# Performance work log

Hardware: AMD Instinct MI355X
Metric: run time of the kernel (lower is better)

## Reference

```python
import jax, jax.numpy as jnp
import numpy as np

SORB = 64      # spin orbitals (sequence length)
NELE = 32      # electrons
H = 512        # num_hiddens
B = 4096       # batch
ALPHA = NELE // 2                      # = beta = 16 (spin-up / spin-down electrons)
MIN_I = min(SORB - 2 * ALPHA, 2 * ALPHA)  # = 32; symmetry mask active for i >= MIN_I
EPS = 1e-12


def setup_inputs() -> dict:
    key = jax.random.key(0)
    ks = jax.random.split(key, 10)
    s_in = 1.0 / np.sqrt(2.0)
    s_h = 1.0 / np.sqrt(H)
    return {
        "x": jax.random.randint(ks[0], (B, SORB), 0, 2, dtype=jnp.int32),  # occupancies {0,1}
        "W_ih0": jax.random.normal(ks[1], (3 * H, 2), jnp.float32) * s_in,   # GRU layer0 input weights (r,z,n)
        "W_hh0": jax.random.normal(ks[2], (3 * H, H), jnp.float32) * s_h,
        "W_ih1": jax.random.normal(ks[3], (3 * H, H), jnp.float32) * s_h,    # GRU layer1
        "W_hh1": jax.random.normal(ks[4], (3 * H, H), jnp.float32) * s_h,
        "W_amp": jax.random.normal(ks[5], (2, H), jnp.float32) * s_h,
        "b_amp": jax.random.normal(ks[6], (2,), jnp.float32) * 0.01,
        "W_phase": jax.random.normal(ks[7], (2, H), jnp.float32) * s_h,
        "b_phase": jax.random.normal(ks[8], (2,), jnp.float32) * 0.01,
    }


def _gru_cell(x_in, h, Wih, Whh):
    # PyTorch GRU (bias=False), gate order r, z, n
    gi = x_in @ Wih.T          # (B, 3H)
    gh = h @ Whh.T             # (B, 3H)
    r = jax.nn.sigmoid(gi[:, :H] + gh[:, :H])
    z = jax.nn.sigmoid(gi[:, H:2 * H] + gh[:, H:2 * H])
    n = jnp.tanh(gi[:, 2 * H:] + r * gh[:, 2 * H:])
    return (1.0 - z) * n + z * h


def reference(x, W_ih0, W_hh0, W_ih1, W_hh1, W_amp, b_amp, W_phase, b_phase):
    dt = W_ih0.dtype
    bits = x.astype(jnp.int32)           # (B, SORB) occupancies
    nb = bits.shape[0]

    def step(carry, inp):
        h0, h1, x0, amp, phase, nup, ndn = carry
        i, b_i = inp                      # site index, occupancy bits (B,)
        h0n = _gru_cell(x0, h0, W_ih0, W_hh0)
        h1n = _gru_cell(h0n, h1, W_ih1, W_hh1)
        y = h1n                           # (B, H)
        # amplitude: sqrt(softmax(linear))
        y_amp = jnp.sqrt(jax.nn.softmax(y @ W_amp.T + b_amp, axis=1))   # (B, 2)
        # phase: pi * softsign(linear)
        ph = y @ W_phase.T + b_phase
        y_ph = jnp.pi * ph / (1.0 + jnp.abs(ph))
        # particle-number symmetry mask (alpha == beta spin sectors)
        is_even = (i % 2) == 0            # even sites: spin-up, odd: spin-down
        cnt = jnp.where(is_even, nup, ndn)
        lower = (ALPHA - SORB // 2 + i // 2).astype(dt)
        occ_ok = (cnt < ALPHA).astype(dt)
        unocc_ok = (cnt > lower).astype(dt)
        mask = jnp.stack([unocc_ok, occ_ok], axis=1)
        masked = y_amp * mask
        masked = masked / jnp.sqrt(jnp.sum(masked * masked, axis=1, keepdims=True) + EPS)
        y_amp = jnp.where(i >= MIN_I, masked, y_amp)
        # accumulate conditional amplitude / phase at the sampled occupancy
        sel_a = jnp.take_along_axis(y_amp, b_i[:, None], axis=1)[:, 0]
        sel_p = jnp.take_along_axis(y_ph, b_i[:, None], axis=1)[:, 0]
        amp = amp * sel_a
        phase = phase + sel_p
        bf = b_i.astype(dt)
        nup = nup + jnp.where(is_even, bf, 0.0)
        ndn = ndn + jnp.where(is_even, 0.0, bf)
        x0n = jax.nn.one_hot(b_i, 2, dtype=dt)  # next-step GRU input
        return (h0n, h1n, x0n, amp, phase, nup, ndn), None

    init = (
        jnp.zeros((nb, H), dt), jnp.zeros((nb, H), dt), jnp.zeros((nb, 2), dt),
        jnp.ones((nb,), dt), jnp.zeros((nb,), dt), jnp.zeros((nb,), dt), jnp.zeros((nb,), dt),
    )
    xs = (jnp.arange(SORB), bits.T)       # scan over sites
    (_, _, _, amp, phase, _, _), _ = jax.lax.scan(step, init, xs)
    # complex wavefunction psi = amp * exp(1j*phase); returned as real pair (amp, phase)
    return jnp.stack([amp, phase], axis=-1)
```

## Files before the change

### kernel.cpp

```cpp
#include <hip/hip_runtime.h>
#include <hip/hip_bf16.h>

#define SORB  64
#define HID   512
#define BATCH 4096
#define N3H   1536
#define KD    512
#define BK    64
#define PI_F  3.14159265358979f

typedef _Float16 half8 __attribute__((ext_vector_type(8)));
typedef float    floatx4 __attribute__((ext_vector_type(4)));

__device__ __forceinline__ void gload16(const void* g, void* l) {
    __builtin_amdgcn_global_load_lds(
        (const __attribute__((address_space(1))) void*)g,
        (__attribute__((address_space(3))) void*)l, 16, 0, 0);
}

__device__ __forceinline__ float sigmoidf_(float x) { return 1.f / (1.f + __expf(-x)); }
__device__ __forceinline__ float tanhf_(float x) {
    x = fminf(fmaxf(x, -15.f), 15.f);
    const float e2 = __expf(2.f * x);
    return (e2 - 1.f) / (e2 + 1.f);
}

__global__ __launch_bounds__(256) void convw_kernel(
    const float* __restrict__ w0, const float* __restrict__ w1, const float* __restrict__ w2,
    _Float16* __restrict__ o0, _Float16* __restrict__ o1, _Float16* __restrict__ o2)
{
    const int i = blockIdx.x * 256 + threadIdx.x;
    if (i < N3H * KD) {
        o0[i] = (_Float16)w0[i];
        o1[i] = (_Float16)w1[i];
        o2[i] = (_Float16)w2[i];
    }
}

__global__ __launch_bounds__(256) void init_kernel(
    float* __restrict__ amp, float* __restrict__ phase,
    int* __restrict__ nup, int* __restrict__ ndn)
{
    const int i = blockIdx.x * 256 + threadIdx.x;
    if (i < BATCH) { amp[i] = 1.f; phase[i] = 0.f; nup[i] = 0; ndn[i] = 0; }
}


__global__ __launch_bounds__(256) void step1_kernel(
    const _Float16* __restrict__ h0h_c, const _Float16* __restrict__ h1h_c,
    const _Float16* __restrict__ wh0,   const _Float16* __restrict__ wh1,
    const float* __restrict__ Wih0, const int* __restrict__ bits,
    float* __restrict__ h0f, _Float16* __restrict__ h0h_n,
    _Float16* __restrict__ gB, int step)
{
    const int z = blockIdx.z;
    const _Float16* A = z ? h1h_c : h0h_c;
    const _Float16* W = z ? wh1 : wh0;
    const int j0 = blockIdx.x * 64;
    const int m0 = blockIdx.y * 64;

    __shared__ __align__(16) _Float16 As[64 * BK];
    __shared__ __align__(16) _Float16 Bs[192 * BK];

    const int tid  = threadIdx.x;
    const int lane = tid & 63;
    const int wid  = tid >> 6;
    const int wm   = wid >> 1, wj = wid & 1;

    floatx4 acc[2][2][3];
    const floatx4 z4 = {0.f, 0.f, 0.f, 0.f};
#pragma unroll
    for (int a = 0; a < 2; ++a)
#pragma unroll
        for (int b = 0; b < 2; ++b)
#pragma unroll
            for (int g = 0; g < 3; ++g) acc[a][b][g] = z4;

    const _Float16* a_srcp[2];
#pragma unroll
    for (int k2 = 0; k2 < 2; ++k2) {
        const int p = tid + k2 * 256, row = p >> 3, c = (p & 7) ^ (row & 7);
        a_srcp[k2] = A + (size_t)(m0 + row) * KD + c * 8;
    }
    const _Float16* b_srcp[6];
#pragma unroll
    for (int k2 = 0; k2 < 6; ++k2) {
        const int p = tid + k2 * 256, row = p >> 3, c = (p & 7) ^ (row & 7);
        const int grow = (row >> 6) * HID + j0 + (row & 63);
        b_srcp[k2] = W + (size_t)grow * KD + c * 8;
    }
    _Float16* a_dst[2];
#pragma unroll
    for (int k2 = 0; k2 < 2; ++k2) a_dst[k2] = As + (size_t)(k2 * 256 + wid * 64) * 8;
    _Float16* b_dst[6];
#pragma unroll
    for (int k2 = 0; k2 < 6; ++k2) b_dst[k2] = Bs + (size_t)(k2 * 256 + wid * 64) * 8;

    const int ku = lane >> 4;
    int aoff[2][2], boff[2][3][2];
#pragma unroll
    for (int mf = 0; mf < 2; ++mf) {
        const int r = wm * 32 + mf * 16 + (lane & 15);
#pragma unroll
        for (int kk = 0; kk < 2; ++kk)
            aoff[mf][kk] = r * BK + (((kk * 4 + ku) ^ (r & 7)) * 8);
    }
#pragma unroll
    for (int jf = 0; jf < 2; ++jf)
#pragma unroll
        for (int g = 0; g < 3; ++g) {
            const int r = g * 64 + wj * 32 + jf * 16 + (lane & 15);
#pragma unroll
            for (int kk = 0; kk < 2; ++kk)
                boff[jf][g][kk] = r * BK + (((kk * 4 + ku) ^ (r & 7)) * 8);
        }

    for (int kt = 0; kt < 8; ++kt) {
        const int k0 = kt * BK;
#pragma unroll
        for (int k2 = 0; k2 < 2; ++k2) gload16(a_srcp[k2] + k0, a_dst[k2]);
#pragma unroll
        for (int k2 = 0; k2 < 6; ++k2) gload16(b_srcp[k2] + k0, b_dst[k2]);
        __syncthreads();
#pragma unroll
        for (int kk = 0; kk < 2; ++kk) {
            half8 af[2], bf[2][3];
#pragma unroll
            for (int mf = 0; mf < 2; ++mf) af[mf] = *(const half8*)(As + aoff[mf][kk]);
#pragma unroll
            for (int jf = 0; jf < 2; ++jf)
#pragma unroll
                for (int g = 0; g < 3; ++g) bf[jf][g] = *(const half8*)(Bs + boff[jf][g][kk]);
#pragma unroll
            for (int mf = 0; mf < 2; ++mf)
#pragma unroll
                for (int jf = 0; jf < 2; ++jf)
#pragma unroll
                    for (int g = 0; g < 3; ++g)
                        acc[mf][jf][g] = __builtin_amdgcn_mfma_f32_16x16x32_f16(af[mf], bf[jf][g], acc[mf][jf][g], 0, 0, 0);
        }
        __syncthreads();
    }

    if (z == 0) {
#pragma unroll
        for (int mf = 0; mf < 2; ++mf)
#pragma unroll
            for (int jf = 0; jf < 2; ++jf) {
                const floatx4 gr = acc[mf][jf][0];
                const floatx4 gz = acc[mf][jf][1];
                const floatx4 gn = acc[mf][jf][2];
#pragma unroll
                for (int reg = 0; reg < 4; ++reg) {
                    const int m = m0 + wm * 32 + mf * 16 + (lane >> 4) * 4 + reg;
                    const int j = j0 + wj * 32 + jf * 16 + (lane & 15);
                    float gir = 0.f, giz = 0.f, gin = 0.f;
                    if (step > 0) {
                        const int t = bits[m * SORB + step - 1];
                        gir = Wih0[j * 2 + t];
                        giz = Wih0[(HID + j) * 2 + t];
                        gin = Wih0[(2 * HID + j) * 2 + t];
                    }
                    const float r  = sigmoidf_(gir + gr[reg]);
                    const float zz = sigmoidf_(giz + gz[reg]);
                    const float n  = tanhf_(gin + r * gn[reg]);
                    const size_t idx = (size_t)m * HID + j;
                    const float h  = h0f[idx];
                    const float hn = (1.f - zz) * n + zz * h;
                    h0f[idx]   = hn;
                    h0h_n[idx] = (_Float16)hn;
                }
            }
    } else {
#pragma unroll
        for (int mf = 0; mf < 2; ++mf)
#pragma unroll
            for (int jf = 0; jf < 2; ++jf)
#pragma unroll
                for (int g = 0; g < 3; ++g)
#pragma unroll
                    for (int reg = 0; reg < 4; ++reg) {
                        const int m = m0 + wm * 32 + mf * 16 + (lane >> 4) * 4 + reg;
                        const int j = j0 + wj * 32 + jf * 16 + (lane & 15);
                        gB[(size_t)m * N3H + g * HID + j] = (_Float16)acc[mf][jf][g][reg];
                    }
    }
}

__global__ __launch_bounds__(256) void step2_kernel(
    const _Float16* __restrict__ h0h_n, const _Float16* __restrict__ wi1,
    const _Float16* __restrict__ gB,
    float* __restrict__ h1f, _Float16* __restrict__ h1h_n)
{
    const int j0 = blockIdx.x * 64;
    const int m0 = blockIdx.y * 64;

    __shared__ __align__(16) _Float16 As[64 * BK];
    __shared__ __align__(16) _Float16 Bs[192 * BK];

    const int tid  = threadIdx.x;
    const int lane = tid & 63;
    const int wid  = tid >> 6;
    const int wm   = wid >> 1, wj = wid & 1;

    floatx4 acc[2][2][3];
    const floatx4 z4 = {0.f, 0.f, 0.f, 0.f};
#pragma unroll
    for (int a = 0; a < 2; ++a)
#pragma unroll
        for (int b = 0; b < 2; ++b)
#pragma unroll
            for (int g = 0; g < 3; ++g) acc[a][b][g] = z4;

    const _Float16* a_srcp[2];
#pragma unroll
    for (int k2 = 0; k2 < 2; ++k2) {
        const int p = tid + k2 * 256, row = p >> 3, c = (p & 7) ^ (row & 7);
        a_srcp[k2] = h0h_n + (size_t)(m0 + row) * KD + c * 8;
    }
    const _Float16* b_srcp[6];
#pragma unroll
    for (int k2 = 0; k2 < 6; ++k2) {
        const int p = tid + k2 * 256, row = p >> 3, c = (p & 7) ^ (row & 7);
        const int grow = (row >> 6) * HID + j0 + (row & 63);
        b_srcp[k2] = wi1 + (size_t)grow * KD + c * 8;
    }
    _Float16* a_dst[2];
#pragma unroll
    for (int k2 = 0; k2 < 2; ++k2) a_dst[k2] = As + (size_t)(k2 * 256 + wid * 64) * 8;
    _Float16* b_dst[6];
#pragma unroll
    for (int k2 = 0; k2 < 6; ++k2) b_dst[k2] = Bs + (size_t)(k2 * 256 + wid * 64) * 8;

    const int ku = lane >> 4;
    int aoff[2][2], boff[2][3][2];
#pragma unroll
    for (int mf = 0; mf < 2; ++mf) {
        const int r = wm * 32 + mf * 16 + (lane & 15);
#pragma unroll
        for (int kk = 0; kk < 2; ++kk)
            aoff[mf][kk] = r * BK + (((kk * 4 + ku) ^ (r & 7)) * 8);
    }
#pragma unroll
    for (int jf = 0; jf < 2; ++jf)
#pragma unroll
        for (int g = 0; g < 3; ++g) {
            const int r = g * 64 + wj * 32 + jf * 16 + (lane & 15);
#pragma unroll
            for (int kk = 0; kk < 2; ++kk)
                boff[jf][g][kk] = r * BK + (((kk * 4 + ku) ^ (r & 7)) * 8);
        }

    for (int kt = 0; kt < 8; ++kt) {
        const int k0 = kt * BK;
#pragma unroll
        for (int k2 = 0; k2 < 2; ++k2) gload16(a_srcp[k2] + k0, a_dst[k2]);
#pragma unroll
        for (int k2 = 0; k2 < 6; ++k2) gload16(b_srcp[k2] + k0, b_dst[k2]);
        __syncthreads();
#pragma unroll
        for (int kk = 0; kk < 2; ++kk) {
            half8 af[2], bf[2][3];
#pragma unroll
            for (int mf = 0; mf < 2; ++mf) af[mf] = *(const half8*)(As + aoff[mf][kk]);
#pragma unroll
            for (int jf = 0; jf < 2; ++jf)
#pragma unroll
                for (int g = 0; g < 3; ++g) bf[jf][g] = *(const half8*)(Bs + boff[jf][g][kk]);
#pragma unroll
            for (int mf = 0; mf < 2; ++mf)
#pragma unroll
                for (int jf = 0; jf < 2; ++jf)
#pragma unroll
                    for (int g = 0; g < 3; ++g)
                        acc[mf][jf][g] = __builtin_amdgcn_mfma_f32_16x16x32_f16(af[mf], bf[jf][g], acc[mf][jf][g], 0, 0, 0);
        }
        __syncthreads();
    }

#pragma unroll
    for (int mf = 0; mf < 2; ++mf)
#pragma unroll
        for (int jf = 0; jf < 2; ++jf) {
            const floatx4 gr = acc[mf][jf][0];
            const floatx4 gz = acc[mf][jf][1];
            const floatx4 gn = acc[mf][jf][2];
#pragma unroll
            for (int reg = 0; reg < 4; ++reg) {
                const int m = m0 + wm * 32 + mf * 16 + (lane >> 4) * 4 + reg;
                const int j = j0 + wj * 32 + jf * 16 + (lane & 15);
                const size_t gbase = (size_t)m * N3H;
                const float ghr = (float)gB[gbase + j];
                const float ghz = (float)gB[gbase + HID + j];
                const float ghn = (float)gB[gbase + 2 * HID + j];
                const float r  = sigmoidf_(gr[reg] + ghr);
                const float zz = sigmoidf_(gz[reg] + ghz);
                const float n  = tanhf_(gn[reg] + r * ghn);
                const size_t idx = (size_t)m * HID + j;
                const float h  = h1f[idx];
                const float hn = (1.f - zz) * n + zz * h;
                h1f[idx]   = hn;
                h1h_n[idx] = (_Float16)hn;
            }
        }
}

__global__ __launch_bounds__(256) void head_kernel(
    const _Float16* __restrict__ h1h_n,
    const float* __restrict__ Wamp, const float* __restrict__ bamp,
    const float* __restrict__ Wph,  const float* __restrict__ bph,
    const int* __restrict__ bits,
    float* __restrict__ amp, float* __restrict__ phase,
    int* __restrict__ nup, int* __restrict__ ndn,
    float* __restrict__ out, int step)
{
    const int lane = threadIdx.x & 63;
    const int m    = blockIdx.x * 4 + (threadIdx.x >> 6);
    const half8 hv = *(const half8*)(h1h_n + (size_t)m * HID + lane * 8);
    float d0 = 0.f, d1 = 0.f, d2 = 0.f, d3 = 0.f;
#pragma unroll
    for (int e = 0; e < 8; ++e) {
        const int j = lane * 8 + e;
        const float hn = (float)hv[e];
        d0 += hn * Wamp[j];       d1 += hn * Wamp[HID + j];
        d2 += hn * Wph[j];        d3 += hn * Wph[HID + j];
    }
#pragma unroll
    for (int off = 1; off < 64; off <<= 1) {
        d0 += __shfl_xor(d0, off); d1 += __shfl_xor(d1, off);
        d2 += __shfl_xor(d2, off); d3 += __shfl_xor(d3, off);
    }
    if (lane == 0) {
        const float a0 = d0 + bamp[0];
        const float a1 = d1 + bamp[1];
        const float mx = fmaxf(a0, a1);
        const float e0 = __expf(a0 - mx), e1 = __expf(a1 - mx);
        const float inv = 1.f / (e0 + e1);
        float ya0 = sqrtf(e0 * inv), ya1 = sqrtf(e1 * inv);
        const float p0 = d2 + bph[0];
        const float p1 = d3 + bph[1];
        const float yp0 = PI_F * p0 / (1.f + fabsf(p0));
        const float yp1 = PI_F * p1 / (1.f + fabsf(p1));
        const int even = ((step & 1) == 0);
        const int cnt = even ? nup[m] : ndn[m];
        if (step >= 32) {
            const int lower = (step >> 1) - 16;
            const float m0v = (cnt > lower) ? ya0 : 0.f;
            const float m1v = (cnt < 16) ? ya1 : 0.f;
            const float nrm = sqrtf(m0v * m0v + m1v * m1v + 1e-12f);
            ya0 = m0v / nrm; ya1 = m1v / nrm;
        }
        const int bi = bits[m * SORB + step];
        const float na = amp[m] * (bi ? ya1 : ya0);
        const float np = phase[m] + (bi ? yp1 : yp0);
        amp[m] = na; phase[m] = np;
        if (bi) { if (even) nup[m] = cnt + 1; else ndn[m] = cnt + 1; }
        if (step == SORB - 1) {
            out[m * 2 + 0] = na;
            out[m * 2 + 1] = np;
        }
    }
}

extern "C" void kernel_launch(void* const* d_in, const int* in_sizes, int n_in,
                              void* d_out, int out_size, void* d_ws, size_t ws_size,
                              hipStream_t stream) {
    const int*   bits = (const int*)d_in[0];
    const float* Wih0 = (const float*)d_in[1];
    const float* Whh0 = (const float*)d_in[2];
    const float* Wih1 = (const float*)d_in[3];
    const float* Whh1 = (const float*)d_in[4];
    const float* Wamp = (const float*)d_in[5];
    const float* bamp = (const float*)d_in[6];
    const float* Wph  = (const float*)d_in[7];
    const float* bph  = (const float*)d_in[8];
    float* out = (float*)d_out;

    char* ws = (char*)d_ws;
    size_t off = 0;
    auto alloc = [&](size_t bytes) {
        void* p = ws + off;
        off = (off + bytes + 255) & ~(size_t)255;
        return p;
    };
    _Float16* wh0 = (_Float16*)alloc((size_t)N3H * KD * 2);
    _Float16* wi1 = (_Float16*)alloc((size_t)N3H * KD * 2);
    _Float16* wh1 = (_Float16*)alloc((size_t)N3H * KD * 2);
    float*    h0f = (float*)alloc((size_t)BATCH * HID * 4);
    float*    h1f = (float*)alloc((size_t)BATCH * HID * 4);
    _Float16* h0hA = (_Float16*)alloc((size_t)BATCH * HID * 2);
    _Float16* h0hB = (_Float16*)alloc((size_t)BATCH * HID * 2);
    _Float16* h1hA = (_Float16*)alloc((size_t)BATCH * HID * 2);
    _Float16* h1hB = (_Float16*)alloc((size_t)BATCH * HID * 2);
    _Float16* gB  = (_Float16*)alloc((size_t)BATCH * N3H * 2);
    float*    amp   = (float*)alloc((size_t)BATCH * 4);
    float*    phase = (float*)alloc((size_t)BATCH * 4);
    int*      nup   = (int*)alloc((size_t)BATCH * 4);
    int*      ndn   = (int*)alloc((size_t)BATCH * 4);

    _Float16* h0h[2] = {h0hA, h0hB};
    _Float16* h1h[2] = {h1hA, h1hB};

    hipMemsetAsync(h0f, 0, (size_t)BATCH * HID * 4, stream);
    hipMemsetAsync(h1f, 0, (size_t)BATCH * HID * 4, stream);
    hipMemsetAsync(h0hA, 0, (size_t)BATCH * HID * 2, stream);
    hipMemsetAsync(h1hA, 0, (size_t)BATCH * HID * 2, stream);
    convw_kernel<<<(N3H * KD + 255) / 256, 256, 0, stream>>>(Whh0, Wih1, Whh1, wh0, wi1, wh1);
    init_kernel<<<BATCH / 256, 256, 0, stream>>>(amp, phase, nup, ndn);

    for (int s = 0; s < SORB; ++s) {
        const int cur = s & 1, nxt = cur ^ 1;
        step1_kernel<<<dim3(8, 64, 2), 256, 0, stream>>>(
            h0h[cur], h1h[cur], wh0, wh1, Wih0, bits, h0f, h0h[nxt], gB, s);
        step2_kernel<<<dim3(8, 64, 1), 256, 0, stream>>>(
            h0h[nxt], wi1, gB, h1f, h1h[nxt]);
        head_kernel<<<BATCH / 4, 256, 0, stream>>>(
            h1h[nxt], Wamp, bamp, Wph, bph, bits, amp, phase, nup, ndn, out, s);
    }
}
```

Before: 3.307 ms.

## Fuse head into next step's GEMM, double-buffer weights, load A directly to registers

The per-step head kernel is folded into the z=1 blocks of the next step1 launch, which process the previous step's h1 rows. A single head launch remains at the end for the last step, which removes one launch per step. The GEMM kernels now double-buffer the weight tile in LDS so the next tile's load overlaps the current MFMAs, and they read the activation operand straight from global memory into registers instead of staging it in LDS. The costs are larger LDS use (two 24KB buffers), which may lower occupancy, and extra epilogue work in the z=1 blocks.

```diff
diff --git a/kernel.cpp b/kernel.cpp
--- a/kernel.cpp
+++ b/kernel.cpp
@@ -45,278 +45,16 @@
     if (i < BATCH) { amp[i] = 1.f; phase[i] = 0.f; nup[i] = 0; ndn[i] = 0; }
 }
 
-
-__global__ __launch_bounds__(256) void step1_kernel(
-    const _Float16* __restrict__ h0h_c, const _Float16* __restrict__ h1h_c,
-    const _Float16* __restrict__ wh0,   const _Float16* __restrict__ wh1,
-    const float* __restrict__ Wih0, const int* __restrict__ bits,
-    float* __restrict__ h0f, _Float16* __restrict__ h0h_n,
-    _Float16* __restrict__ gB, int step)
-{
-    const int z = blockIdx.z;
-    const _Float16* A = z ? h1h_c : h0h_c;
-    const _Float16* W = z ? wh1 : wh0;
-    const int j0 = blockIdx.x * 64;
-    const int m0 = blockIdx.y * 64;
-
-    __shared__ __align__(16) _Float16 As[64 * BK];
-    __shared__ __align__(16) _Float16 Bs[192 * BK];
-
-    const int tid  = threadIdx.x;
-    const int lane = tid & 63;
-    const int wid  = tid >> 6;
-    const int wm   = wid >> 1, wj = wid & 1;
-
-    floatx4 acc[2][2][3];
-    const floatx4 z4 = {0.f, 0.f, 0.f, 0.f};
-#pragma unroll
-    for (int a = 0; a < 2; ++a)
-#pragma unroll
-        for (int b = 0; b < 2; ++b)
-#pragma unroll
-            for (int g = 0; g < 3; ++g) acc[a][b][g] = z4;
-
-    const _Float16* a_srcp[2];
-#pragma unroll
-    for (int k2 = 0; k2 < 2; ++k2) {
-        const int p = tid + k2 * 256, row = p >> 3, c = (p & 7) ^ (row & 7);
-        a_srcp[k2] = A + (size_t)(m0 + row) * KD + c * 8;
-    }
-    const _Float16* b_srcp[6];
-#pragma unroll
-    for (int k2 = 0; k2 < 6; ++k2) {
-        const int p = tid + k2 * 256, row = p >> 3, c = (p & 7) ^ (row & 7);
-        const int grow = (row >> 6) * HID + j0 + (row & 63);
-        b_srcp[k2] = W + (size_t)grow * KD + c * 8;
-    }
-    _Float16* a_dst[2];
-#pragma unroll
-    for (int k2 = 0; k2 < 2; ++k2) a_dst[k2] = As + (size_t)(k2 * 256 + wid * 64) * 8;
-    _Float16* b_dst[6];
-#pragma unroll
-    for (int k2 = 0; k2 < 6; ++k2) b_dst[k2] = Bs + (size_t)(k2 * 256 + wid * 64) * 8;
-
-    const int ku = lane >> 4;
-    int aoff[2][2], boff[2][3][2];
-#pragma unroll
-    for (int mf = 0; mf < 2; ++mf) {
-        const int r = wm * 32 + mf * 16 + (lane & 15);
-#pragma unroll
-        for (int kk = 0; kk < 2; ++kk)
-            aoff[mf][kk] = r * BK + (((kk * 4 + ku) ^ (r & 7)) * 8);
-    }
-#pragma unroll
-    for (int jf = 0; jf < 2; ++jf)
-#pragma unroll
-        for (int g = 0; g < 3; ++g) {
-            const int r = g * 64 + wj * 32 + jf * 16 + (lane & 15);
-#pragma unroll
-            for (int kk = 0; kk < 2; ++kk)
-                boff[jf][g][kk] = r * BK + (((kk * 4 + ku) ^ (r & 7)) * 8);
-        }
-
-    for (int kt = 0; kt < 8; ++kt) {
-        const int k0 = kt * BK;
-#pragma unroll
-        for (int k2 = 0; k2 < 2; ++k2) gload16(a_srcp[k2] + k0, a_dst[k2]);
-#pragma unroll
-        for (int k2 = 0; k2 < 6; ++k2) gload16(b_srcp[k2] + k0, b_dst[k2]);
-        __syncthreads();
-#pragma unroll
-        for (int kk = 0; kk < 2; ++kk) {
-            half8 af[2], bf[2][3];
-#pragma unroll
-            for (int mf = 0; mf < 2; ++mf) af[mf] = *(const half8*)(As + aoff[mf][kk]);
-#pragma unroll
-            for (int jf = 0; jf < 2; ++jf)
-#pragma unroll
-                for (int g = 0; g < 3; ++g) bf[jf][g] = *(const half8*)(Bs + boff[jf][g][kk]);
-#pragma unroll
-            for (int mf = 0; mf < 2; ++mf)
-#pragma unroll
-                for (int jf = 0; jf < 2; ++jf)
-#pragma unroll
-                    for (int g = 0; g < 3; ++g)
-                        acc[mf][jf][g] = __builtin_amdgcn_mfma_f32_16x16x32_f16(af[mf], bf[jf][g], acc[mf][jf][g], 0, 0, 0);
-        }
-        __syncthreads();
-    }
-
-    if (z == 0) {
-#pragma unroll
-        for (int mf = 0; mf < 2; ++mf)
-#pragma unroll
-            for (int jf = 0; jf < 2; ++jf) {
-                const floatx4 gr = acc[mf][jf][0];
-                const floatx4 gz = acc[mf][jf][1];
-                const floatx4 gn = acc[mf][jf][2];
-#pragma unroll
-                for (int reg = 0; reg < 4; ++reg) {
-                    const int m = m0 + wm * 32 + mf * 16 + (lane >> 4) * 4 + reg;
-                    const int j = j0 + wj * 32 + jf * 16 + (lane & 15);
-                    float gir = 0.f, giz = 0.f, gin = 0.f;
-                    if (step > 0) {
-                        const int t = bits[m * SORB + step - 1];
-                        gir = Wih0[j * 2 + t];
-                        giz = Wih0[(HID + j) * 2 + t];
-                        gin = Wih0[(2 * HID + j) * 2 + t];
-                    }
-                    const float r  = sigmoidf_(gir + gr[reg]);
-                    const float zz = sigmoidf_(giz + gz[reg]);
-                    const float n  = tanhf_(gin + r * gn[reg]);
-                    const size_t idx = (size_t)m * HID + j;
-                    const float h  = h0f[idx];
-                    const float hn = (1.f - zz) * n + zz * h;
-                    h0f[idx]   = hn;
-                    h0h_n[idx] = (_Float16)hn;
-                }
-            }
-    } else {
-#pragma unroll
-        for (int mf = 0; mf < 2; ++mf)
-#pragma unroll
-            for (int jf = 0; jf < 2; ++jf)
-#pragma unroll
-                for (int g = 0; g < 3; ++g)
-#pragma unroll
-                    for (int reg = 0; reg < 4; ++reg) {
-                        const int m = m0 + wm * 32 + mf * 16 + (lane >> 4) * 4 + reg;
-                        const int j = j0 + wj * 32 + jf * 16 + (lane & 15);
-                        gB[(size_t)m * N3H + g * HID + j] = (_Float16)acc[mf][jf][g][reg];
-                    }
-    }
-}
-
-__global__ __launch_bounds__(256) void step2_kernel(
-    const _Float16* __restrict__ h0h_n, const _Float16* __restrict__ wi1,
-    const _Float16* __restrict__ gB,
-    float* __restrict__ h1f, _Float16* __restrict__ h1h_n)
-{
-    const int j0 = blockIdx.x * 64;
-    const int m0 = blockIdx.y * 64;
-
-    __shared__ __align__(16) _Float16 As[64 * BK];
-    __shared__ __align__(16) _Float16 Bs[192 * BK];
-
-    const int tid  = threadIdx.x;
-    const int lane = tid & 63;
-    const int wid  = tid >> 6;
-    const int wm   = wid >> 1, wj = wid & 1;
-
-    floatx4 acc[2][2][3];
-    const floatx4 z4 = {0.f, 0.f, 0.f, 0.f};
-#pragma unroll
-    for (int a = 0; a < 2; ++a)
-#pragma unroll
-        for (int b = 0; b < 2; ++b)
-#pragma unroll
-            for (int g = 0; g < 3; ++g) acc[a][b][g] = z4;
-
-    const _Float16* a_srcp[2];
-#pragma unroll
-    for (int k2 = 0; k2 < 2; ++k2) {
-        const int p = tid + k2 * 256, row = p >> 3, c = (p & 7) ^ (row & 7);
-        a_srcp[k2] = h0h_n + (size_t)(m0 + row) * KD + c * 8;
-    }
-    const _Float16* b_srcp[6];
-#pragma unroll
-    for (int k2 = 0; k2 < 6; ++k2) {
-        const int p = tid + k2 * 256, row = p >> 3, c = (p & 7) ^ (row & 7);
-        const int grow = (row >> 6) * HID + j0 + (row & 63);
-        b_srcp[k2] = wi1 + (size_t)grow * KD + c * 8;
-    }
-    _Float16* a_dst[2];
-#pragma unroll
-    for (int k2 = 0; k2 < 2; ++k2) a_dst[k2] = As + (size_t)(k2 * 256 + wid * 64) * 8;
-    _Float16* b_dst[6];
-#pragma unroll
-    for (int k2 = 0; k2 < 6; ++k2) b_dst[k2] = Bs + (size_t)(k2 * 256 + wid * 64) * 8;
-
-    const int ku = lane >> 4;
-    int aoff[2][2], boff[2][3][2];
-#pragma unroll
-    for (int mf = 0; mf < 2; ++mf) {
-        const int r = wm * 32 + mf * 16 + (lane & 15);
-#pragma unroll
-        for (int kk = 0; kk < 2; ++kk)
-            aoff[mf][kk] = r * BK + (((kk * 4 + ku) ^ (r & 7)) * 8);
-    }
-#pragma unroll
-    for (int jf = 0; jf < 2; ++jf)
-#pragma unroll
-        for (int g = 0; g < 3; ++g) {
-            const int r = g * 64 + wj * 32 + jf * 16 + (lane & 15);
-#pragma unroll
-            for (int kk = 0; kk < 2; ++kk)
-                boff[jf][g][kk] = r * BK + (((kk * 4 + ku) ^ (r & 7)) * 8);
-        }
-
-    for (int kt = 0; kt < 8; ++kt) {
-        const int k0 = kt * BK;
-#pragma unroll
-        for (int k2 = 0; k2 < 2; ++k2) gload16(a_srcp[k2] + k0, a_dst[k2]);
-#pragma unroll
-        for (int k2 = 0; k2 < 6; ++k2) gload16(b_srcp[k2] + k0, b_dst[k2]);
-        __syncthreads();
-#pragma unroll
-        for (int kk = 0; kk < 2; ++kk) {
-            half8 af[2], bf[2][3];
-#pragma unroll
-            for (int mf = 0; mf < 2; ++mf) af[mf] = *(const half8*)(As + aoff[mf][kk]);
-#pragma unroll
-            for (int jf = 0; jf < 2; ++jf)
-#pragma unroll
-                for (int g = 0; g < 3; ++g) bf[jf][g] = *(const half8*)(Bs + boff[jf][g][kk]);
-#pragma unroll
-            for (int mf = 0; mf < 2; ++mf)
-#pragma unroll
-                for (int jf = 0; jf < 2; ++jf)
-#pragma unroll
-                    for (int g = 0; g < 3; ++g)
-                        acc[mf][jf][g] = __builtin_amdgcn_mfma_f32_16x16x32_f16(af[mf], bf[jf][g], acc[mf][jf][g], 0, 0, 0);
-        }
-        __syncthreads();
-    }
-
-#pragma unroll
-    for (int mf = 0; mf < 2; ++mf)
-#pragma unroll
-        for (int jf = 0; jf < 2; ++jf) {
-            const floatx4 gr = acc[mf][jf][0];
-            const floatx4 gz = acc[mf][jf][1];
-            const floatx4 gn = acc[mf][jf][2];
-#pragma unroll
-            for (int reg = 0; reg < 4; ++reg) {
-                const int m = m0 + wm * 32 + mf * 16 + (lane >> 4) * 4 + reg;
-                const int j = j0 + wj * 32 + jf * 16 + (lane & 15);
-                const size_t gbase = (size_t)m * N3H;
-                const float ghr = (float)gB[gbase + j];
-                const float ghz = (float)gB[gbase + HID + j];
-                const float ghn = (float)gB[gbase + 2 * HID + j];
-                const float r  = sigmoidf_(gr[reg] + ghr);
-                const float zz = sigmoidf_(gz[reg] + ghz);
-                const float n  = tanhf_(gn[reg] + r * ghn);
-                const size_t idx = (size_t)m * HID + j;
-                const float h  = h1f[idx];
-                const float hn = (1.f - zz) * n + zz * h;
-                h1f[idx]   = hn;
-                h1h_n[idx] = (_Float16)hn;
-            }
-        }
-}
-
-__global__ __launch_bounds__(256) void head_kernel(
-    const _Float16* __restrict__ h1h_n,
+__device__ __forceinline__ void head_row(
+    const _Float16* __restrict__ h1, int m,
     const float* __restrict__ Wamp, const float* __restrict__ bamp,
     const float* __restrict__ Wph,  const float* __restrict__ bph,
     const int* __restrict__ bits,
     float* __restrict__ amp, float* __restrict__ phase,
     int* __restrict__ nup, int* __restrict__ ndn,
-    float* __restrict__ out, int step)
-{
-    const int lane = threadIdx.x & 63;
-    const int m    = blockIdx.x * 4 + (threadIdx.x >> 6);
-    const half8 hv = *(const half8*)(h1h_n + (size_t)m * HID + lane * 8);
+    float* __restrict__ out, int step, int lane)
+{
+    const half8 hv = *(const half8*)(h1 + (size_t)m * HID + lane * 8);
     float d0 = 0.f, d1 = 0.f, d2 = 0.f, d3 = 0.f;
 #pragma unroll
     for (int e = 0; e < 8; ++e) {
@@ -360,6 +98,296 @@
             out[m * 2 + 1] = np;
         }
     }
+}
+
+__global__ __launch_bounds__(256) void step1_kernel(
+    const _Float16* __restrict__ h0h_c, const _Float16* __restrict__ h1h_c,
+    const _Float16* __restrict__ wh0,   const _Float16* __restrict__ wh1,
+    const float* __restrict__ Wih0, const int* __restrict__ bits,
+    float* __restrict__ h0f, _Float16* __restrict__ h0h_n,
+    _Float16* __restrict__ gB, int step,
+    const float* __restrict__ Wamp, const float* __restrict__ bamp,
+    const float* __restrict__ Wph,  const float* __restrict__ bph,
+    float* __restrict__ amp, float* __restrict__ phase,
+    int* __restrict__ nup, int* __restrict__ ndn, float* __restrict__ out)
+{
+    const int z = blockIdx.z;
+    const _Float16* Aop = z ? h1h_c : h0h_c;
+    const _Float16* Wop = z ? wh1 : wh0;
+    const int j0 = blockIdx.x * 64;
+    const int m0 = blockIdx.y * 64;
+
+    __shared__ __align__(16) _Float16 Bs[2][192 * BK];
+
+    const int tid  = threadIdx.x;
+    const int lane = tid & 63;
+    const int wid  = tid >> 6;
+    const int wm   = wid >> 1, wj = wid & 1;
+    const int ku   = lane >> 4;
+
+    floatx4 acc[2][2][3];
+    const floatx4 z4 = {0.f, 0.f, 0.f, 0.f};
+#pragma unroll
+    for (int a = 0; a < 2; ++a)
+#pragma unroll
+        for (int b = 0; b < 2; ++b)
+#pragma unroll
+            for (int g = 0; g < 3; ++g) acc[a][b][g] = z4;
+
+    const _Float16* b_srcp[6];
+#pragma unroll
+    for (int k2 = 0; k2 < 6; ++k2) {
+        const int p = tid + k2 * 256, row = p >> 3, c = (p & 7) ^ (row & 7);
+        const int grow = (row >> 6) * HID + j0 + (row & 63);
+        b_srcp[k2] = Wop + (size_t)grow * KD + c * 8;
+    }
+    _Float16* b_dst0[6];
+    _Float16* b_dst1[6];
+#pragma unroll
+    for (int k2 = 0; k2 < 6; ++k2) {
+        b_dst0[k2] = Bs[0] + (size_t)(k2 * 256 + wid * 64) * 8;
+        b_dst1[k2] = Bs[1] + (size_t)(k2 * 256 + wid * 64) * 8;
+    }
+
+    const _Float16* a_row[2];
+#pragma unroll
+    for (int mf = 0; mf < 2; ++mf)
+        a_row[mf] = Aop + (size_t)(m0 + wm * 32 + mf * 16 + (lane & 15)) * KD + ku * 8;
+
+    int boff[2][3][2];
+#pragma unroll
+    for (int jf = 0; jf < 2; ++jf)
+#pragma unroll
+        for (int g = 0; g < 3; ++g) {
+            const int r = g * 64 + wj * 32 + jf * 16 + (lane & 15);
+#pragma unroll
+            for (int kk = 0; kk < 2; ++kk)
+                boff[jf][g][kk] = r * BK + (((kk * 4 + ku) ^ (r & 7)) * 8);
+        }
+
+#pragma unroll
+    for (int k2 = 0; k2 < 6; ++k2) gload16(b_srcp[k2], b_dst0[k2]);
+    __syncthreads();
+
+#pragma unroll
+    for (int kt = 0; kt < 8; ++kt) {
+        half8 af[2][2];
+#pragma unroll
+        for (int mf = 0; mf < 2; ++mf)
+#pragma unroll
+            for (int kk = 0; kk < 2; ++kk)
+                af[mf][kk] = *(const half8*)(a_row[mf] + kt * BK + kk * 32);
+        if (kt < 7) {
+#pragma unroll
+            for (int k2 = 0; k2 < 6; ++k2)
+                gload16(b_srcp[k2] + (kt + 1) * BK, ((kt & 1) ? b_dst0 : b_dst1)[k2]);
+        }
+        const _Float16* Bcur = Bs[kt & 1];
+#pragma unroll
+        for (int kk = 0; kk < 2; ++kk) {
+            half8 bf[2][3];
+#pragma unroll
+            for (int jf = 0; jf < 2; ++jf)
+#pragma unroll
+                for (int g = 0; g < 3; ++g) bf[jf][g] = *(const half8*)(Bcur + boff[jf][g][kk]);
+#pragma unroll
+            for (int mf = 0; mf < 2; ++mf)
+#pragma unroll
+                for (int jf = 0; jf < 2; ++jf)
+#pragma unroll
+                    for (int g = 0; g < 3; ++g)
+                        acc[mf][jf][g] = __builtin_amdgcn_mfma_f32_16x16x32_f16(
+                            af[mf][kk], bf[jf][g], acc[mf][jf][g], 0, 0, 0);
+        }
+        __syncthreads();
+    }
+
+    if (z == 0) {
+#pragma unroll
+        for (int mf = 0; mf < 2; ++mf)
+#pragma unroll
+            for (int jf = 0; jf < 2; ++jf) {
+                const floatx4 gr = acc[mf][jf][0];
+                const floatx4 gz = acc[mf][jf][1];
+                const floatx4 gn = acc[mf][jf][2];
+#pragma unroll
+                for (int reg = 0; reg < 4; ++reg) {
+                    const int m = m0 + wm * 32 + mf * 16 + (lane >> 4) * 4 + reg;
+                    const int j = j0 + wj * 32 + jf * 16 + (lane & 15);
+                    float gir = 0.f, giz = 0.f, gin = 0.f;
+                    if (step > 0) {
+                        const int tb = bits[m * SORB + step - 1];
+                        gir = Wih0[j * 2 + tb];
+                        giz = Wih0[(HID + j) * 2 + tb];
+                        gin = Wih0[(2 * HID + j) * 2 + tb];
+                    }
+                    const float r  = sigmoidf_(gir + gr[reg]);
+                    const float zz = sigmoidf_(giz + gz[reg]);
+                    const float n  = tanhf_(gin + r * gn[reg]);
+                    const size_t idx = (size_t)m * HID + j;
+                    const float h  = h0f[idx];
+                    const float hn = (1.f - zz) * n + zz * h;
+                    h0f[idx]   = hn;
+                    h0h_n[idx] = (_Float16)hn;
+                }
+            }
+    } else {
+#pragma unroll
+        for (int mf = 0; mf < 2; ++mf)
+#pragma unroll
+            for (int jf = 0; jf < 2; ++jf)
+#pragma unroll
+                for (int g = 0; g < 3; ++g)
+#pragma unroll
+                    for (int reg = 0; reg < 4; ++reg) {
+                        const int m = m0 + wm * 32 + mf * 16 + (lane >> 4) * 4 + reg;
+                        const int j = j0 + wj * 32 + jf * 16 + (lane & 15);
+                        gB[(size_t)m * N3H + g * HID + j] = (_Float16)acc[mf][jf][g][reg];
+                    }
+        if (step > 0) {
+            const int bid = blockIdx.y * 8 + blockIdx.x;
+#pragma unroll
+            for (int rr = 0; rr < 2; ++rr) {
+                const int m = bid * 8 + wid * 2 + rr;
+                head_row(h1h_c, m, Wamp, bamp, Wph, bph, bits,
+                         amp, phase, nup, ndn, out, step - 1, lane);
+            }
+        }
+    }
+}
+
+__global__ __launch_bounds__(256) void step2_kernel(
+    const _Float16* __restrict__ h0h_n, const _Float16* __restrict__ wi1,
+    const _Float16* __restrict__ gB,
+    float* __restrict__ h1f, _Float16* __restrict__ h1h_n)
+{
+    const int j0 = blockIdx.x * 64;
+    const int m0 = blockIdx.y * 64;
+
+    __shared__ __align__(16) _Float16 Bs[2][192 * BK];
+
+    const int tid  = threadIdx.x;
+    const int lane = tid & 63;
+    const int wid  = tid >> 6;
+    const int wm   = wid >> 1, wj = wid & 1;
+    const int ku   = lane >> 4;
+
+    floatx4 acc[2][2][3];
+    const floatx4 z4 = {0.f, 0.f, 0.f, 0.f};
+#pragma unroll
+    for (int a = 0; a < 2; ++a)
+#pragma unroll
+        for (int b = 0; b < 2; ++b)
+#pragma unroll
+            for (int g = 0; g < 3; ++g) acc[a][b][g] = z4;
+
+    const _Float16* b_srcp[6];
+#pragma unroll
+    for (int k2 = 0; k2 < 6; ++k2) {
+        const int p = tid + k2 * 256, row = p >> 3, c = (p & 7) ^ (row & 7);
+        const int grow = (row >> 6) * HID + j0 + (row & 63);
+        b_srcp[k2] = wi1 + (size_t)grow * KD + c * 8;
+    }
+    _Float16* b_dst0[6];
+    _Float16* b_dst1[6];
+#pragma unroll
+    for (int k2 = 0; k2 < 6; ++k2) {
+        b_dst0[k2] = Bs[0] + (size_t)(k2 * 256 + wid * 64) * 8;
+        b_dst1[k2] = Bs[1] + (size_t)(k2 * 256 + wid * 64) * 8;
+    }
+
+    const _Float16* a_row[2];
+#pragma unroll
+    for (int mf = 0; mf < 2; ++mf)
+        a_row[mf] = h0h_n + (size_t)(m0 + wm * 32 + mf * 16 + (lane & 15)) * KD + ku * 8;
+
+    int boff[2][3][2];
+#pragma unroll
+    for (int jf = 0; jf < 2; ++jf)
+#pragma unroll
+        for (int g = 0; g < 3; ++g) {
+            const int r = g * 64 + wj * 32 + jf * 16 + (lane & 15);
+#pragma unroll
+            for (int kk = 0; kk < 2; ++kk)
+                boff[jf][g][kk] = r * BK + (((kk * 4 + ku) ^ (r & 7)) * 8);
+        }
+
+#pragma unroll
+    for (int k2 = 0; k2 < 6; ++k2) gload16(b_srcp[k2], b_dst0[k2]);
+    __syncthreads();
+
+#pragma unroll
+    for (int kt = 0; kt < 8; ++kt) {
+        half8 af[2][2];
+#pragma unroll
+        for (int mf = 0; mf < 2; ++mf)
+#pragma unroll
+            for (int kk = 0; kk < 2; ++kk)
+                af[mf][kk] = *(const half8*)(a_row[mf] + kt * BK + kk * 32);
+        if (kt < 7) {
+#pragma unroll
+            for (int k2 = 0; k2 < 6; ++k2)
+                gload16(b_srcp[k2] + (kt + 1) * BK, ((kt & 1) ? b_dst0 : b_dst1)[k2]);
+        }
+        const _Float16* Bcur = Bs[kt & 1];
+#pragma unroll
+        for (int kk = 0; kk < 2; ++kk) {
+            half8 bf[2][3];
+#pragma unroll
+            for (int jf = 0; jf < 2; ++jf)
+#pragma unroll
+                for (int g = 0; g < 3; ++g) bf[jf][g] = *(const half8*)(Bcur + boff[jf][g][kk]);
+#pragma unroll
+            for (int mf = 0; mf < 2; ++mf)
+#pragma unroll
+                for (int jf = 0; jf < 2; ++jf)
+#pragma unroll
+                    for (int g = 0; g < 3; ++g)
+                        acc[mf][jf][g] = __builtin_amdgcn_mfma_f32_16x16x32_f16(
+                            af[mf][kk], bf[jf][g], acc[mf][jf][g], 0, 0, 0);
+        }
+        __syncthreads();
+    }
+
+#pragma unroll
+    for (int mf = 0; mf < 2; ++mf)
+#pragma unroll
+        for (int jf = 0; jf < 2; ++jf) {
+            const floatx4 gr = acc[mf][jf][0];
+            const floatx4 gz = acc[mf][jf][1];
+            const floatx4 gn = acc[mf][jf][2];
+#pragma unroll
+            for (int reg = 0; reg < 4; ++reg) {
+                const int m = m0 + wm * 32 + mf * 16 + (lane >> 4) * 4 + reg;
+                const int j = j0 + wj * 32 + jf * 16 + (lane & 15);
+                const size_t gbase = (size_t)m * N3H;
+                const float ghr = (float)gB[gbase + j];
+                const float ghz = (float)gB[gbase + HID + j];
+                const float ghn = (float)gB[gbase + 2 * HID + j];
+                const float r  = sigmoidf_(gr[reg] + ghr);
+                const float zz = sigmoidf_(gz[reg] + ghz);
+                const float n  = tanhf_(gn[reg] + r * ghn);
+                const size_t idx = (size_t)m * HID + j;
+                const float h  = h1f[idx];
+                const float hn = (1.f - zz) * n + zz * h;
+                h1f[idx]   = hn;
+                h1h_n[idx] = (_Float16)hn;
+            }
+        }
+}
+
+__global__ __launch_bounds__(256) void head_kernel(
+    const _Float16* __restrict__ h1h_n,
+    const float* __restrict__ Wamp, const float* __restrict__ bamp,
+    const float* __restrict__ Wph,  const float* __restrict__ bph,
+    const int* __restrict__ bits,
+    float* __restrict__ amp, float* __restrict__ phase,
+    int* __restrict__ nup, int* __restrict__ ndn,
+    float* __restrict__ out, int step)
+{
+    const int lane = threadIdx.x & 63;
+    const int m    = blockIdx.x * 4 + (threadIdx.x >> 6);
+    head_row(h1h_n, m, Wamp, bamp, Wph, bph, bits, amp, phase, nup, ndn, out, step, lane);
 }
 
 extern "C" void kernel_launch(void* const* d_in, const int* in_sizes, int n_in,
@@ -411,10 +439,11 @@
     for (int s = 0; s < SORB; ++s) {
         const int cur = s & 1, nxt = cur ^ 1;
         step1_kernel<<<dim3(8, 64, 2), 256, 0, stream>>>(
-            h0h[cur], h1h[cur], wh0, wh1, Wih0, bits, h0f, h0h[nxt], gB, s);
+            h0h[cur], h1h[cur], wh0, wh1, Wih0, bits, h0f, h0h[nxt], gB, s,
+            Wamp, bamp, Wph, bph, amp, phase, nup, ndn, out);
         step2_kernel<<<dim3(8, 64, 1), 256, 0, stream>>>(
             h0h[nxt], wi1, gB, h1f, h1h[nxt]);
-        head_kernel<<<BATCH / 4, 256, 0, stream>>>(
-            h1h[nxt], Wamp, bamp, Wph, bph, bits, amp, phase, nup, ndn, out, s);
-    }
-}
+    }
+    head_kernel<<<BATCH / 4, 256, 0, stream>>>(
+        h1h[0], Wamp, bamp, Wph, bph, bits, amp, phase, nup, ndn, out, SORB - 1);
+}
```

New measurement: 4.071 ms. 23.1% more time.
